# Kernel optimization log

Hardware: AMD Instinct MI355X
Metric: run time of the kernel (lower is better)

The kernel has to match this reference:

```python
import jax, jax.numpy as jnp
import numpy as np

B, T, E, H, FF = 8, 1024, 1024, 16, 4096
HD = E // H
SCALE = HD ** -0.5
EPS = 1e-12  # LayerNorm eps from TransformerLayer


def layer_norm(x, w, b):
    u = x.mean(-1, keepdims=True)
    s = ((x - u) ** 2).mean(-1, keepdims=True)  # biased variance, as in module
    return w * (x - u) / jnp.sqrt(s + EPS) + b


def setup_inputs() -> dict:
    key = jax.random.key(0)
    ks = jax.random.split(key, 8)
    std = 0.02  # nn.init.normal_(std=0.02)
    x = jax.random.normal(ks[0], (B, T, E), jnp.float32)
    # padding mask: positions >= length are padding (1 = ignore); ensure no all-masked row
    lengths = jax.random.randint(ks[1], (B,), T // 2, T + 1)
    self_padding_mask = jnp.arange(T)[None, :] >= lengths[:, None]
    # causal mask from SelfAttentionMask: triu(ones, 1)
    attn_mask = jnp.triu(jnp.ones((T, T), dtype=bool), 1)
    in_w = std * jax.random.normal(ks[2], (3 * E, E), jnp.float32)
    in_b = jnp.zeros((3 * E,), jnp.float32)
    out_w = std * jax.random.normal(ks[3], (E, E), jnp.float32)
    out_b = jnp.zeros((E,), jnp.float32)
    fc1_w = std * jax.random.normal(ks[4], (FF, E), jnp.float32)
    fc1_b = jnp.zeros((FF,), jnp.float32)
    fc2_w = std * jax.random.normal(ks[5], (E, FF), jnp.float32)
    fc2_b = jnp.zeros((E,), jnp.float32)
    ln1_w = jnp.ones((E,), jnp.float32)
    ln1_b = jnp.zeros((E,), jnp.float32)
    ln2_w = jnp.ones((E,), jnp.float32)
    ln2_b = jnp.zeros((E,), jnp.float32)
    return dict(x=x, in_w=in_w, in_b=in_b, out_w=out_w, out_b=out_b,
                fc1_w=fc1_w, fc1_b=fc1_b, fc2_w=fc2_w, fc2_b=fc2_b,
                ln1_w=ln1_w, ln1_b=ln1_b, ln2_w=ln2_w, ln2_b=ln2_b,
                self_padding_mask=self_padding_mask, attn_mask=attn_mask)


def reference(x, in_w, in_b, out_w, out_b, fc1_w, fc1_b, fc2_w, fc2_b,
              ln1_w, ln1_b, ln2_w, ln2_b, self_padding_mask, attn_mask):
    b, t, e = x.shape
    # --- self attention sublayer ---
    residual = x
    qkv = x @ in_w.T + in_b                       # [B,T,3E] fused in_proj (qkv_same path)
    q, k, v = jnp.split(qkv, 3, axis=-1)
    q = (q * SCALE).reshape(b, t, H, HD)
    k = k.reshape(b, t, H, HD)
    v = v.reshape(b, t, H, HD)
    scores = jnp.einsum('bqhd,bkhd->bhqk', q, k)  # [B,H,T,T]
    mask = attn_mask[None, None, :, :] | self_padding_mask[:, None, None, :]
    scores = jnp.where(mask, -jnp.inf, scores)
    p = jax.nn.softmax(scores, axis=-1)
    attn = jnp.einsum('bhqk,bkhd->bqhd', p, v).reshape(b, t, e)
    attn = attn @ out_w.T + out_b
    x = layer_norm(residual + attn, ln1_w, ln1_b)
    # --- feed-forward sublayer ---
    residual = x
    h = jax.nn.relu(x @ fc1_w.T + fc1_b)
    x = layer_norm(residual + (h @ fc2_w.T + fc2_b), ln2_w, ln2_b)
    return x
```

## Files before the change

### kernel.cpp

```cpp
#include <hip/hip_runtime.h>

typedef unsigned short u16;
typedef __attribute__((ext_vector_type(8))) short short8;
typedef __attribute__((ext_vector_type(4))) short short4v;
typedef __attribute__((ext_vector_type(4))) float f32x4;

#define DEV static __device__ __forceinline__

DEV float bf2f(u16 h) {
    union { unsigned int u; float f; } v; v.u = ((unsigned int)h) << 16; return v.f;
}
DEV u16 f2bf(float f) {
    union { float f; unsigned int u; } v; v.f = f;
    unsigned int r = (v.u + 0x7fff + ((v.u >> 16) & 1)) >> 16;
    return (u16)r;
}
DEV float ldx(const void* p, size_t i, int f32) {
    return f32 ? ((const float*)p)[i] : bf2f(((const u16*)p)[i]);
}

#define GLD16(g, l) __builtin_amdgcn_global_load_lds( \
    (const __attribute__((address_space(1))) void*)(g), \
    (__attribute__((address_space(3))) void*)(l), 16, 0, 0)

#define STAGE(P, pf32, eoff, dst8) do {                                        \
    if (!(pf32)) { GLD16(((const u16*)(P)) + (eoff), (dst8)); }                \
    else {                                                                     \
        const float* _p = ((const float*)(P)) + (eoff);                        \
        f32x4 _a = *(const f32x4*)_p, _b = *(const f32x4*)(_p + 4);            \
        short8 _s;                                                             \
        _s[0]=(short)f2bf(_a[0]); _s[1]=(short)f2bf(_a[1]);                    \
        _s[2]=(short)f2bf(_a[2]); _s[3]=(short)f2bf(_a[3]);                    \
        _s[4]=(short)f2bf(_b[0]); _s[5]=(short)f2bf(_b[1]);                    \
        _s[6]=(short)f2bf(_b[2]); _s[7]=(short)f2bf(_b[3]);                    \
        *(short8*)(dst8) = _s;                                                 \
    } } while (0)

__global__ __launch_bounds__(64) void probe_kernel(
    const void* __restrict__ x, const void* __restrict__ pad,
    int* __restrict__ flags, int* __restrict__ flagsA)
{
    const int lane = threadIdx.x;
    const u16* xu = (const u16*)x;
    const unsigned int e = (xu[lane * 2] >> 7) & 0xFF;
    const int sane = (e >= 0x70 && e <= 0x8F) ? 1 : 0;
    unsigned long long m = __ballot(sane);
    const int f32 = (__popcll(m) < 32) ? 1 : 0;

    const unsigned int* pi = (const unsigned int*)pad;
    int bytes = 0;
#pragma unroll
    for (int j = 0; j < 6; j++) {
        unsigned int v = pi[128 + j * 64 + lane];
        if (v > 1u) bytes = 1;
    }
    m = __ballot(bytes);
    if (lane == 0) {
        flags[0] = f32; flags[1] = (m != 0ULL) ? 1 : 0;
        flagsA[0] = 0;  flagsA[1] = 0;
    }
}

__global__ __launch_bounds__(256) void conv4(
    const void* __restrict__ src, u16* __restrict__ dst, int n4,
    const int* __restrict__ flags)
{
    const int i = blockIdx.x * 256 + threadIdx.x;
    if (i >= n4) return;
    if (flags[0]) {
        f32x4 v = ((const f32x4*)src)[i];
        short4v s;
        s[0] = (short)f2bf(v[0]); s[1] = (short)f2bf(v[1]);
        s[2] = (short)f2bf(v[2]); s[3] = (short)f2bf(v[3]);
        ((short4v*)dst)[i] = s;
    } else {
        ((short4v*)dst)[i] = ((const short4v*)src)[i];
    }
}

__global__ __launch_bounds__(256) void mask_to_bias(
    const void* __restrict__ pad, float* __restrict__ out,
    const int* __restrict__ flags)
{
    const int i = blockIdx.x * 256 + threadIdx.x;
    const int mv = flags[1] ? (int)((const unsigned char*)pad)[i]
                            : ((const int*)pad)[i];
    out[i] = mv ? -1e30f : 0.0f;
}

#define GEMM_CORE(Av, ASEL, a_row0, Wv, w_off, ldw, K)                        \
    __shared__ __align__(16) u16 As[128 * 32];                                \
    __shared__ __align__(16) u16 Bs[128 * 32];                                \
    const int inf32 = flags[0];                                               \
    const int af32  = (ASEL) ? inf32 : 0;                                     \
    const int tid  = threadIdx.x;                                             \
    const int lane = tid & 63;                                                \
    const int wave = tid >> 6;                                                \
    const int lc   = lane & 15;                                               \
    const int quad = lane >> 4;                                               \
    const int m0 = blockIdx.x * 128;                                          \
    const int n0 = blockIdx.y * 128;                                          \
    const int wm = (wave >> 1) * 64;                                          \
    const int wn = (wave & 1) * 64;                                           \
    const int r0 = tid >> 2;                                                  \
    const int ko = (tid & 3) * 8;                                             \
    f32x4 acc[4][4] = {};                                                     \
    for (int k0 = 0; k0 < (K); k0 += 32) {                                    \
        STAGE(Av, af32, ((size_t)(a_row0) + m0 + r0) * (K) + k0 + ko,         \
              &As[tid * 8]);                                                  \
        STAGE(Av, af32, ((size_t)(a_row0) + m0 + r0 + 64) * (K) + k0 + ko,    \
              &As[2048 + tid * 8]);                                           \
        STAGE(Wv, inf32, (size_t)(w_off) + (size_t)(n0 + r0) * (ldw) + k0 + ko,\
              &Bs[tid * 8]);                                                  \
        STAGE(Wv, inf32, (size_t)(w_off) + (size_t)(n0 + r0 + 64) * (ldw) + k0 + ko,\
              &Bs[2048 + tid * 8]);                                           \
        __syncthreads();                                                      \
        short8 afr[4], bfr[4];                                                \
        const int qd = quad * 8;                                              \
        _Pragma("unroll")                                                     \
        for (int mt = 0; mt < 4; mt++)                                        \
            afr[mt] = *(const short8*)&As[(wm + mt * 16 + lc) * 32 + qd];     \
        _Pragma("unroll")                                                     \
        for (int nt = 0; nt < 4; nt++)                                        \
            bfr[nt] = *(const short8*)&Bs[(wn + nt * 16 + lc) * 32 + qd];     \
        _Pragma("unroll")                                                     \
        for (int mt = 0; mt < 4; mt++)                                        \
            _Pragma("unroll")                                                 \
            for (int nt = 0; nt < 4; nt++)                                    \
                acc[mt][nt] = __builtin_amdgcn_mfma_f32_16x16x32_bf16(        \
                    afr[mt], bfr[nt], acc[mt][nt], 0, 0, 0);                  \
        __syncthreads();                                                      \
    }                                                                         \
    const int ce0 = n0 + wn + lc;                                             \
    const int re0 = m0 + wm + quad * 4;

template<int EPI>
__global__ __launch_bounds__(256, 2) void gemm_bt(
    const void* __restrict__ A, int a_sel, long a_row0,
    const void* __restrict__ W, long w_off,
    const void* __restrict__ bias, long b_off,
    const void* __restrict__ resid, int r_sel, long r_row0,
    u16* __restrict__ C, long c_row0,
    int N, int K, int ldw, const int* __restrict__ flags)
{
    GEMM_CORE(A, a_sel, a_row0, W, w_off, ldw, K)
    const int rf32 = r_sel ? inf32 : 0;
#pragma unroll
    for (int mt = 0; mt < 4; mt++) {
#pragma unroll
        for (int nt = 0; nt < 4; nt++) {
            const int c = ce0 + nt * 16;
            const float bv = ldx(bias, (size_t)b_off + c, inf32);
#pragma unroll
            for (int i = 0; i < 4; i++) {
                const int r = re0 + mt * 16 + i;
                float v = acc[mt][nt][i] + bv;
                if (EPI == 1)
                    v += ldx(resid, ((size_t)r_row0 + r) * N + c, rf32);
                if (EPI == 2) v = fmaxf(v, 0.0f);
                C[((size_t)c_row0 + r) * N + c] = f2bf(v);
            }
        }
    }
}

__global__ __launch_bounds__(256, 2) void gemm_qkv(
    const void* __restrict__ A, long a_row0,
    const void* __restrict__ W, const void* __restrict__ bias,
    u16* __restrict__ Qo, u16* __restrict__ Ko, u16* __restrict__ Vt,
    const int* __restrict__ flags)
{
    GEMM_CORE(A, 1, a_row0, W, 0, 1024, 1024)
    if (n0 < 1024) {
#pragma unroll
        for (int mt = 0; mt < 4; mt++)
#pragma unroll
            for (int nt = 0; nt < 4; nt++) {
                const int c = ce0 + nt * 16;
                const float bv = ldx(bias, c, inf32);
#pragma unroll
                for (int i = 0; i < 4; i++) {
                    const int r = re0 + mt * 16 + i;
                    Qo[((size_t)a_row0 + r) * 1024 + c] =
                        f2bf((acc[mt][nt][i] + bv) * 0.125f);
                }
            }
    } else if (n0 < 2048) {
#pragma unroll
        for (int mt = 0; mt < 4; mt++)
#pragma unroll
            for (int nt = 0; nt < 4; nt++) {
                const int c = ce0 + nt * 16;
                const float bv = ldx(bias, c, inf32);
#pragma unroll
                for (int i = 0; i < 4; i++) {
                    const int r = re0 + mt * 16 + i;
                    Ko[(size_t)r * 1024 + (c - 1024)] = f2bf(acc[mt][nt][i] + bv);
                }
            }
    } else {
#pragma unroll
        for (int mt = 0; mt < 4; mt++)
#pragma unroll
            for (int nt = 0; nt < 4; nt++) {
                const int c = ce0 + nt * 16;
                const float bv = ldx(bias, c, inf32);
                const int cv = c - 2048;
                const int hh = cv >> 6, d = cv & 63;
                const int rb = re0 + mt * 16;
                const int bl = rb >> 10, t = rb & 1023;
                short4v pk;
#pragma unroll
                for (int i = 0; i < 4; i++)
                    pk[i] = (short)f2bf(acc[mt][nt][i] + bv);
                *(short4v*)&Vt[((size_t)(bl * 16 + hh) * 64 + d) * 1024 + t] = pk;
            }
    }
}

__global__ __launch_bounds__(256, 2) void gemm_accf32(
    const void* __restrict__ A, const void* __restrict__ W, long w_off,
    const void* __restrict__ bias, const u16* __restrict__ resid, long r_row0,
    float* __restrict__ C, int ldw, int init, const int* __restrict__ flags)
{
    GEMM_CORE(A, 0, 0, W, w_off, ldw, 1024)
#pragma unroll
    for (int mt = 0; mt < 4; mt++) {
#pragma unroll
        for (int nt = 0; nt < 4; nt++) {
            const int c = ce0 + nt * 16;
            const float bv = ldx(bias, c, inf32);
#pragma unroll
            for (int i = 0; i < 4; i++) {
                const int r = re0 + mt * 16 + i;
                float v = acc[mt][nt][i];
                if (init) v += bv + bf2f(resid[((size_t)r_row0 + r) * 1024 + c]);
                else      v += C[(size_t)r * 1024 + c];
                C[(size_t)r * 1024 + c] = v;
            }
        }
    }
}

__global__ __launch_bounds__(256, 2) void attn_kernel(
    u16* __restrict__ QO, const u16* __restrict__ Ko,
    const u16* __restrict__ Vt, const float* __restrict__ kb, int b0)
{
    __shared__ __align__(16) u16 Qs[2 * 128 * 32];
    __shared__ __align__(16) u16 Ks[2][2 * 64 * 32];
    __shared__ __align__(16) u16 Vs[2][2 * 64 * 32];
    __shared__ __align__(16) u16 Ps[4][32 * 72];
    __shared__ float kba[1024];

    const int tid  = threadIdx.x;
    const int lane = tid & 63;
    const int w    = tid >> 6;
    const int lc   = lane & 15;
    const int quad = lane >> 4;
    const int bl = blockIdx.y >> 4;
    const int h  = blockIdx.y & 15;
    const int b  = b0 + bl;

    *(f32x4*)&kba[tid * 4] = *(const f32x4*)&kb[b * 1024 + tid * 4];

    for (int p = 0; p < 2; p++) {
        const int qt = p ? 7 - (int)blockIdx.x : (int)blockIdx.x;

#pragma unroll
        for (int it = 0; it < 4; it++) {
            const int kcd = it >> 1, half = it & 1;
            const int r = half * 64 + (tid >> 2);
            const int c = kcd * 32 + (tid & 3) * 8;
            GLD16(&QO[((size_t)(b * 1024 + qt * 128 + r)) * 1024 + h * 64 + c],
                  &Qs[kcd * 4096 + half * 2048 + tid * 8]);
        }
        {
            const int rr = tid >> 2;
#pragma unroll
            for (int it = 0; it < 2; it++) {
                const int cc = it * 32 + (tid & 3) * 8;
                GLD16(&Ko[((size_t)(bl * 1024 + rr)) * 1024 + h * 64 + cc],
                      &Ks[0][it * 2048 + tid * 8]);
                GLD16(&Vt[((size_t)(bl * 16 + h) * 64 + rr) * 1024 + cc],
                      &Vs[0][it * 2048 + tid * 8]);
            }
        }
        __syncthreads();

        short8 aq[2][2];
#pragma unroll
        for (int mt = 0; mt < 2; mt++)
#pragma unroll
            for (int kc = 0; kc < 2; kc++)
                aq[mt][kc] = *(const short8*)
                    &Qs[kc * 4096 + (w * 32 + mt * 16 + lc) * 32 + quad * 8];

        f32x4 o[2][4] = {};
        float m_i[2][4], l_i[2][4];
#pragma unroll
        for (int mt = 0; mt < 2; mt++)
#pragma unroll
            for (int i = 0; i < 4; i++) { m_i[mt][i] = -1e30f; l_i[mt][i] = 0.0f; }

        const int ktmax = 2 * qt + 2;
        for (int kt = 0; kt < ktmax; kt++) {
            const int cur = kt & 1;
            if (kt + 1 < ktmax) {
                const int nxt = cur ^ 1;
                const int rr = tid >> 2;
#pragma unroll
                for (int it = 0; it < 2; it++) {
                    const int cc = it * 32 + (tid & 3) * 8;
                    GLD16(&Ko[((size_t)(bl * 1024 + (kt + 1) * 64 + rr)) * 1024 + h * 64 + cc],
                          &Ks[nxt][it * 2048 + tid * 8]);
                    GLD16(&Vt[((size_t)(bl * 16 + h) * 64 + rr) * 1024 + (kt + 1) * 64 + cc],
                          &Vs[nxt][it * 2048 + tid * 8]);
                }
            }

            short8 bk[4][2];
#pragma unroll
            for (int nt = 0; nt < 4; nt++)
#pragma unroll
                for (int kc = 0; kc < 2; kc++)
                    bk[nt][kc] = *(const short8*)
                        &Ks[cur][kc * 2048 + (nt * 16 + lc) * 32 + quad * 8];

            f32x4 s[2][4];
#pragma unroll
            for (int mt = 0; mt < 2; mt++)
#pragma unroll
                for (int nt = 0; nt < 4; nt++) {
                    f32x4 z = {};
#pragma unroll
                    for (int kc = 0; kc < 2; kc++)
                        z = __builtin_amdgcn_mfma_f32_16x16x32_bf16(
                            aq[mt][kc], bk[nt][kc], z, 0, 0, 0);
                    s[mt][nt] = z;
                }

            const int causal = (kt >= 2 * qt);
            float al[2][4];
#pragma unroll
            for (int mt = 0; mt < 2; mt++) {
                const int qg0 = qt * 128 + w * 32 + mt * 16 + quad * 4;
#pragma unroll
                for (int nt = 0; nt < 4; nt++) {
                    const int kg = kt * 64 + nt * 16 + lc;
                    const float kbv = kba[kt * 64 + nt * 16 + lc];
#pragma unroll
                    for (int i = 0; i < 4; i++) {
                        float sv = s[mt][nt][i] + kbv;
                        if (causal && kg > qg0 + i) sv = -1e30f;
                        s[mt][nt][i] = sv;
                    }
                }
                float mnew[4], rs[4];
#pragma unroll
                for (int i = 0; i < 4; i++) {
                    float rm = fmaxf(fmaxf(s[mt][0][i], s[mt][1][i]),
                                     fmaxf(s[mt][2][i], s[mt][3][i]));
                    rm = fmaxf(rm, __shfl_xor(rm, 1));
                    rm = fmaxf(rm, __shfl_xor(rm, 2));
                    rm = fmaxf(rm, __shfl_xor(rm, 4));
                    rm = fmaxf(rm, __shfl_xor(rm, 8));
                    mnew[i] = fmaxf(m_i[mt][i], rm);
                    al[mt][i] = exp2f((m_i[mt][i] - mnew[i]) * 1.442695041f);
                    rs[i] = 0.0f;
                }
#pragma unroll
                for (int nt = 0; nt < 4; nt++)
#pragma unroll
                    for (int i = 0; i < 4; i++) {
                        float pp = exp2f((s[mt][nt][i] - mnew[i]) * 1.442695041f);
                        s[mt][nt][i] = pp;
                        rs[i] += pp;
                    }
#pragma unroll
                for (int i = 0; i < 4; i++) {
                    float r = rs[i];
                    r += __shfl_xor(r, 1);
                    r += __shfl_xor(r, 2);
                    r += __shfl_xor(r, 4);
                    r += __shfl_xor(r, 8);
                    l_i[mt][i] = l_i[mt][i] * al[mt][i] + r;
                    m_i[mt][i] = mnew[i];
                }
#pragma unroll
                for (int nt = 0; nt < 4; nt++)
#pragma unroll
                    for (int i = 0; i < 4; i++)
                        Ps[w][(mt * 16 + quad * 4 + i) * 72 + nt * 16 + lc] =
                            f2bf(s[mt][nt][i]);
            }

            short8 ap[2][2], bv2[4][2];
#pragma unroll
            for (int mt = 0; mt < 2; mt++)
#pragma unroll
                for (int kc = 0; kc < 2; kc++)
                    ap[mt][kc] = *(const short8*)
                        &Ps[w][(mt * 16 + lc) * 72 + kc * 32 + quad * 8];
#pragma unroll
            for (int nt = 0; nt < 4; nt++)
#pragma unroll
                for (int kc = 0; kc < 2; kc++)
                    bv2[nt][kc] = *(const short8*)
                        &Vs[cur][kc * 2048 + (nt * 16 + lc) * 32 + quad * 8];
#pragma unroll
            for (int mt = 0; mt < 2; mt++)
#pragma unroll
                for (int nt = 0; nt < 4; nt++) {
                    f32x4 oo = o[mt][nt];
#pragma unroll
                    for (int i = 0; i < 4; i++) oo[i] *= al[mt][i];
#pragma unroll
                    for (int kc = 0; kc < 2; kc++)
                        oo = __builtin_amdgcn_mfma_f32_16x16x32_bf16(
                            ap[mt][kc], bv2[nt][kc], oo, 0, 0, 0);
                    o[mt][nt] = oo;
                }
            __syncthreads();
        }

#pragma unroll
        for (int mt = 0; mt < 2; mt++)
#pragma unroll
            for (int i = 0; i < 4; i++) {
                const float inv = l_i[mt][i] > 0.0f ? 1.0f / l_i[mt][i] : 0.0f;
#pragma unroll
                for (int nt = 0; nt < 4; nt++) {
                    const int r = qt * 128 + w * 32 + mt * 16 + quad * 4 + i;
                    const int d = nt * 16 + lc;
                    QO[((size_t)(b * 1024 + r)) * 1024 + h * 64 + d] =
                        f2bf(o[mt][nt][i] * inv);
                }
            }
    }
}

template<int IN16, int OUTSEL>
__global__ __launch_bounds__(256) void ln_kernel(
    const void* __restrict__ yv, const void* __restrict__ w,
    const void* __restrict__ bb, void* __restrict__ o, long o_row0,
    const int* __restrict__ flags)
{
    const int row = blockIdx.x;
    const int tid = threadIdx.x;
    const int inf32 = flags[0];
    float x0, x1, x2, x3;
    if (IN16) {
        const u16* p = (const u16*)yv + (size_t)row * 1024 + tid * 4;
        short4v v = *(const short4v*)p;
        x0 = bf2f((u16)v[0]); x1 = bf2f((u16)v[1]);
        x2 = bf2f((u16)v[2]); x3 = bf2f((u16)v[3]);
    } else {
        const float* p = (const float*)yv + (size_t)row * 1024 + tid * 4;
        f32x4 v = *(const f32x4*)p;
        x0 = v[0]; x1 = v[1]; x2 = v[2]; x3 = v[3];
    }
    float s = x0 + x1 + x2 + x3;
    float q = x0 * x0 + x1 * x1 + x2 * x2 + x3 * x3;
#pragma unroll
    for (int off = 32; off; off >>= 1) {
        s += __shfl_xor(s, off);
        q += __shfl_xor(q, off);
    }
    __shared__ float sm[8];
    const int lane = tid & 63, wv = tid >> 6;
    if (lane == 0) { sm[wv] = s; sm[4 + wv] = q; }
    __syncthreads();
    const float ts = sm[0] + sm[1] + sm[2] + sm[3];
    const float tq = sm[4] + sm[5] + sm[6] + sm[7];
    const float mean = ts * (1.0f / 1024.0f);
    float var = tq * (1.0f / 1024.0f) - mean * mean;
    if (var < 0.0f) var = 0.0f;
    const float rinv = rsqrtf(var + 1e-12f);

    const size_t obase = ((size_t)o_row0 + row) * 1024 + tid * 4;
#pragma unroll
    for (int j = 0; j < 4; j++) {
        const int c = tid * 4 + j;
        float xv = (j == 0) ? x0 : (j == 1) ? x1 : (j == 2) ? x2 : x3;
        float v = ldx(w, c, inf32) * ((xv - mean) * rinv) + ldx(bb, c, inf32);
        if (OUTSEL && inf32) ((float*)o)[obase + j] = v;
        else                 ((u16*)o)[obase + j] = f2bf(v);
    }
}

extern "C" void kernel_launch(void* const* d_in, const int* in_sizes, int n_in,
                              void* d_out, int out_size, void* d_ws, size_t ws_size,
                              hipStream_t stream)
{
    const void* x     = d_in[0];
    const void* in_w  = d_in[1];
    const void* in_b  = d_in[2];
    const void* out_w = d_in[3];
    const void* out_b = d_in[4];
    const void* fc1_w = d_in[5];
    const void* fc1_b = d_in[6];
    const void* fc2_w = d_in[7];
    const void* fc2_b = d_in[8];
    const void* ln1w  = d_in[9];
    const void* ln1b  = d_in[10];
    const void* ln2w  = d_in[11];
    const void* ln2b  = d_in[12];
    const void* pad   = d_in[13];
    u16* outp = (u16*)d_out;
    char* ws = (char*)d_ws;
    dim3 blk(256);

    const size_t MB = 1024 * 1024;
    const bool bigWS = ws_size >= (105 * MB + 64 * 1024);

    if (bigWS) {
        u16*   xb   = (u16*)(ws + 0);
        u16*   x1   = (u16*)(ws + 0);
        u16*   w1b  = (u16*)(ws + 16 * MB);
        u16*   wob  = (u16*)(ws + 22 * MB);
        u16*   f1b  = (u16*)(ws + 24 * MB);
        u16*   f2b  = (u16*)(ws + 32 * MB);
        u16*   inbb = (u16*)(ws + 40 * MB);
        u16*   outbb= (u16*)(ws + 40 * MB + 8192);
        u16*   f1bb = (u16*)(ws + 40 * MB + 16384);
        u16*   f2bb = (u16*)(ws + 40 * MB + 24576);
        u16*   Ko   = (u16*)(ws + 41 * MB);
        u16*   Vt   = (u16*)(ws + 57 * MB);
        u16*   y1   = (u16*)(ws + 73 * MB);
        u16*   h    = (u16*)(ws + 41 * MB);
        u16*   y2   = (u16*)(ws + 16 * MB);
        int*   flags  = (int*)(ws + 105 * MB);
        int*   flagsA = (int*)(ws + 105 * MB + 32);
        float* kbias  = (float*)(ws + 105 * MB + 64);

        probe_kernel<<<dim3(1), dim3(64), 0, stream>>>(x, pad, flags, flagsA);
        mask_to_bias<<<dim3(32), blk, 0, stream>>>(pad, kbias, flags);
        conv4<<<dim3(8192), blk, 0, stream>>>(x, xb, 2097152, flags);
        conv4<<<dim3(3072), blk, 0, stream>>>(in_w, w1b, 786432, flags);
        conv4<<<dim3(1024), blk, 0, stream>>>(out_w, wob, 262144, flags);
        conv4<<<dim3(4096), blk, 0, stream>>>(fc1_w, f1b, 1048576, flags);
        conv4<<<dim3(4096), blk, 0, stream>>>(fc2_w, f2b, 1048576, flags);
        conv4<<<dim3(3), blk, 0, stream>>>(in_b, inbb, 768, flags);
        conv4<<<dim3(1), blk, 0, stream>>>(out_b, outbb, 256, flags);
        conv4<<<dim3(4), blk, 0, stream>>>(fc1_b, f1bb, 1024, flags);
        conv4<<<dim3(1), blk, 0, stream>>>(fc2_b, f2bb, 256, flags);

        gemm_qkv<<<dim3(64, 24), blk, 0, stream>>>(
            xb, 0, w1b, inbb, outp, Ko, Vt, flagsA);
        attn_kernel<<<dim3(4, 128), blk, 0, stream>>>(outp, Ko, Vt, kbias, 0);
        gemm_bt<1><<<dim3(64, 8), blk, 0, stream>>>(
            outp, 0, 0, wob, 0, outbb, 0, xb, 0, 0, y1, 0, 1024, 1024, 1024, flagsA);
        ln_kernel<1, 0><<<dim3(8192), blk, 0, stream>>>(y1, ln1w, ln1b, x1, 0, flags);
        gemm_bt<2><<<dim3(64, 32), blk, 0, stream>>>(
            x1, 0, 0, f1b, 0, f1bb, 0, nullptr, 0, 0, h, 0, 4096, 1024, 1024, flagsA);
        gemm_bt<1><<<dim3(64, 8), blk, 0, stream>>>(
            h, 0, 0, f2b, 0, f2bb, 0, x1, 0, 0, y2, 0, 1024, 4096, 4096, flagsA);
        ln_kernel<1, 1><<<dim3(8192), blk, 0, stream>>>(y2, ln2w, ln2b, d_out, 0, flags);
    } else {
        u16*   Ko    = (u16*)(ws + 0);
        u16*   Vt    = (u16*)(ws + 4 * MB);
        u16*   y1h   = (u16*)(ws + 0);
        float* acc   = (float*)(ws + 0);
        u16*   hc    = (u16*)(ws + 8 * MB);
        int*   flags  = (int*)(ws + 12 * MB);
        int*   flagsA = (int*)(ws + 12 * MB + 32);
        float* kbias  = (float*)(ws + 12 * MB + 64);

        probe_kernel<<<dim3(1), dim3(64), 0, stream>>>(x, pad, flags, flagsA);
        mask_to_bias<<<dim3(32), blk, 0, stream>>>(pad, kbias, flags);

        for (int q = 0; q < 4; q++) {
            const long r0 = (long)q * 2048;
            gemm_qkv<<<dim3(16, 24), blk, 0, stream>>>(
                x, r0, in_w, in_b, outp, Ko, Vt, flags);
            attn_kernel<<<dim3(4, 32), blk, 0, stream>>>(
                outp, Ko, Vt, kbias, q * 2);
        }
        for (int hf = 0; hf < 2; hf++) {
            const long r0 = (long)hf * 4096;
            gemm_bt<1><<<dim3(32, 8), blk, 0, stream>>>(
                outp, 0, r0, out_w, 0, out_b, 0, x, 1, r0,
                y1h, 0, 1024, 1024, 1024, flags);
            ln_kernel<1, 0><<<dim3(4096), blk, 0, stream>>>(
                y1h, ln1w, ln1b, outp, r0, flags);
        }
        for (int q = 3; q >= 0; q--) {
            const long r0 = (long)q * 2048;
            for (int c = 0; c < 4; c++) {
                gemm_bt<2><<<dim3(16, 8), blk, 0, stream>>>(
                    outp, 0, r0, fc1_w, (long)c * 1024 * 1024, fc1_b, (long)c * 1024,
                    nullptr, 0, 0, hc, 0, 1024, 1024, 1024, flags);
                gemm_accf32<<<dim3(16, 8), blk, 0, stream>>>(
                    hc, fc2_w, (long)c * 1024, fc2_b, outp, r0,
                    acc, 4096, c == 0, flags);
            }
            ln_kernel<0, 1><<<dim3(2048), blk, 0, stream>>>(
                acc, ln2w, ln2b, d_out, r0, flags);
        }
    }
}
```

Measured before the change: 611.2 us.

## Add 256x256-tile 8-wave pipelined GEMM for out-proj and FFN layers

Adds a new bf16 GEMM kernel with 512 threads, 256x256 output tiles, double-buffered direct global-to-LDS loads, swizzled LDS reads, barrier-interleaved MFMA phases and s_setprio scheduling. It replaces the previous 128-tile gemm_bt for the output projection and both FFN GEMMs on the big-workspace path. Larger tiles raise arithmetic intensity and cut global traffic, but the grid drops to 128 blocks for the N=1024 GEMMs, which may underfill the 256 CUs. The new kernel also ignores the dtype flags that gemm_bt took, so it assumes bf16 inputs.

After: 580.1 us. 5.1% less time.

```diff
diff --git a/kernel.cpp b/kernel.cpp
--- a/kernel.cpp
+++ b/kernel.cpp
@@ -242,6 +242,117 @@
     }
 }
 
+template<int EPI>
+__global__ __launch_bounds__(512, 2) void gemm8(
+    const u16* __restrict__ A, const u16* __restrict__ W,
+    const u16* __restrict__ bias, const u16* __restrict__ resid,
+    u16* __restrict__ C, int N, int K)
+{
+    __shared__ __align__(16) u16 As8[2][2][8192];
+    __shared__ __align__(16) u16 Bs8[2][2][8192];
+    const int tid  = threadIdx.x;
+    const int lane = tid & 63;
+    const int lc   = lane & 15;
+    const int quad = lane >> 4;
+    const int w    = tid >> 6;
+    const int wr   = w >> 2;
+    const int wc   = w & 3;
+    const int m0 = blockIdx.x * 256;
+    const int n0 = blockIdx.y * 256;
+
+    const int sr   = tid >> 2;
+    const int scol = ((((tid & 3) << 4) ^ (((tid >> 3) & 3) << 4)) >> 1);
+    const size_t aoff0 = (size_t)(m0 + sr) * K + scol;
+    const size_t aoff1 = (size_t)(m0 + 128 + sr) * K + scol;
+    const size_t boff0 = (size_t)(n0 + sr) * K + scol;
+    const size_t boff1 = (size_t)(n0 + 128 + sr) * K + scol;
+
+    const int fsw   = (quad ^ ((lc >> 1) & 3)) << 3;
+    const int aBase = (wr * 128 + lc) * 32 + fsw;
+    const int bBase = (wc * 64 + lc) * 32 + fsw;
+
+#define SA8(buf, kc, tb) do { \
+    GLD16(A + aoff0 + (tb) + (kc) * 32, &As8[buf][kc][tid * 8]); \
+    GLD16(A + aoff1 + (tb) + (kc) * 32, &As8[buf][kc][4096 + tid * 8]); } while (0)
+#define SB8(buf, kc, tb) do { \
+    GLD16(W + boff0 + (tb) + (kc) * 32, &Bs8[buf][kc][tid * 8]); \
+    GLD16(W + boff1 + (tb) + (kc) * 32, &Bs8[buf][kc][4096 + tid * 8]); } while (0)
+#define LDA4(KC, MH) do { _Pragma("unroll") \
+    for (int q_ = 0; q_ < 4; q_++) \
+        af[q_] = *(const short8*)&As8[c][KC][aBase + ((MH) * 4 + q_) * 512]; } while (0)
+#define LDB4(KC) do { _Pragma("unroll") \
+    for (int q_ = 0; q_ < 4; q_++) \
+        bf[q_] = *(const short8*)&Bs8[c][KC][bBase + q_ * 512]; } while (0)
+#define MFMA16(MH) do { _Pragma("unroll") \
+    for (int mq = 0; mq < 4; mq++) { _Pragma("unroll") \
+    for (int nq = 0; nq < 4; nq++) \
+        acc[(MH) * 4 + mq][nq] = __builtin_amdgcn_mfma_f32_16x16x32_bf16( \
+            af[mq], bf[nq], acc[(MH) * 4 + mq][nq], 0, 0, 0); } } while (0)
+#define BARW do { __builtin_amdgcn_s_barrier(); \
+    asm volatile("s_waitcnt lgkmcnt(0)" ::: "memory"); \
+    __builtin_amdgcn_s_setprio(1); } while (0)
+#define BARE do { __builtin_amdgcn_s_setprio(0); \
+    __builtin_amdgcn_s_barrier(); } while (0)
+
+    f32x4 acc[8][4] = {};
+    short8 af[4], bf[4];
+    const int NT = K >> 6;
+
+    SA8(0, 0, 0); SB8(0, 0, 0); SA8(0, 1, 0); SB8(0, 1, 0);
+    if (NT > 1) { SA8(1, 0, 64); SB8(1, 0, 64); }
+    if (NT > 1) asm volatile("s_waitcnt vmcnt(4)" ::: "memory");
+    else        asm volatile("s_waitcnt vmcnt(0)" ::: "memory");
+    __builtin_amdgcn_s_barrier();
+
+    for (int t = 0; t < NT; ++t) {
+        const int c = t & 1, nx = c ^ 1;
+        const int k0 = t << 6;
+        const bool s1 = (t + 1 < NT), s2 = (t + 2 < NT);
+        LDA4(0, 0); LDB4(0);
+        if (s1) SA8(nx, 1, k0 + 64);
+        BARW; MFMA16(0); BARE;
+        LDA4(0, 1);
+        if (s1) SB8(nx, 1, k0 + 64);
+        BARW; MFMA16(1); BARE;
+        LDA4(1, 0); LDB4(1);
+        if (s2) SA8(c, 0, k0 + 128);
+        BARW; MFMA16(0); BARE;
+        LDA4(1, 1);
+        if (s2) SB8(c, 0, k0 + 128);
+        BARW; MFMA16(1);
+        __builtin_amdgcn_s_setprio(0);
+        if (s2) asm volatile("s_waitcnt vmcnt(4)" ::: "memory");
+        else    asm volatile("s_waitcnt vmcnt(0)" ::: "memory");
+        __builtin_amdgcn_s_barrier();
+    }
+
+    const int cb0 = n0 + wc * 64 + lc;
+    const int rb0 = m0 + wr * 128 + quad * 4;
+#pragma unroll
+    for (int mt = 0; mt < 8; mt++) {
+#pragma unroll
+        for (int nt = 0; nt < 4; nt++) {
+            const int cN = cb0 + nt * 16;
+            const float bv = bf2f(bias[cN]);
+#pragma unroll
+            for (int i = 0; i < 4; i++) {
+                const int rM = rb0 + mt * 16 + i;
+                float v = acc[mt][nt][i] + bv;
+                if (EPI == 1) v += bf2f(resid[(size_t)rM * N + cN]);
+                if (EPI == 2) v = fmaxf(v, 0.0f);
+                C[(size_t)rM * N + cN] = f2bf(v);
+            }
+        }
+    }
+#undef SA8
+#undef SB8
+#undef LDA4
+#undef LDB4
+#undef MFMA16
+#undef BARW
+#undef BARE
+}
+
 __global__ __launch_bounds__(256, 2) void attn_kernel(
     u16* __restrict__ QO, const u16* __restrict__ Ko,
     const u16* __restrict__ Vt, const float* __restrict__ kb, int b0)
@@ -509,6 +620,7 @@
     u16* outp = (u16*)d_out;
     char* ws = (char*)d_ws;
     dim3 blk(256);
+    dim3 blk8(512);
 
     const size_t MB = 1024 * 1024;
     const bool bigWS = ws_size >= (105 * MB + 64 * 1024);
@@ -548,13 +660,13 @@
         gemm_qkv<<<dim3(64, 24), blk, 0, stream>>>(
             xb, 0, w1b, inbb, outp, Ko, Vt, flagsA);
         attn_kernel<<<dim3(4, 128), blk, 0, stream>>>(outp, Ko, Vt, kbias, 0);
-        gemm_bt<1><<<dim3(64, 8), blk, 0, stream>>>(
-            outp, 0, 0, wob, 0, outbb, 0, xb, 0, 0, y1, 0, 1024, 1024, 1024, flagsA);
+        gemm8<1><<<dim3(32, 4), blk8, 0, stream>>>(
+            outp, wob, outbb, xb, y1, 1024, 1024);
         ln_kernel<1, 0><<<dim3(8192), blk, 0, stream>>>(y1, ln1w, ln1b, x1, 0, flags);
-        gemm_bt<2><<<dim3(64, 32), blk, 0, stream>>>(
-            x1, 0, 0, f1b, 0, f1bb, 0, nullptr, 0, 0, h, 0, 4096, 1024, 1024, flagsA);
-        gemm_bt<1><<<dim3(64, 8), blk, 0, stream>>>(
-            h, 0, 0, f2b, 0, f2bb, 0, x1, 0, 0, y2, 0, 1024, 4096, 4096, flagsA);
+        gemm8<2><<<dim3(32, 16), blk8, 0, stream>>>(
+            x1, f1b, f1bb, nullptr, h, 4096, 1024);
+        gemm8<1><<<dim3(32, 4), blk8, 0, stream>>>(
+            h, f2b, f2bb, x1, y2, 1024, 4096);
         ln_kernel<1, 1><<<dim3(8192), blk, 0, stream>>>(y2, ln2w, ln2b, d_out, 0, flags);
     } else {
         u16*   Ko    = (u16*)(ws + 0);
```

## Add 512-thread 128x256 triple-buffered bf16 GEMM for projection and FFN layers

Applied to the files above, without the earlier changes.

Introduces a new GEMM kernel family (gemm8, gemm8_qkv) using 8 waves per block, a 128x256 output tile, 64-wide K steps and a three-stage LDS ring filled by direct global-to-LDS loads. Each K step is split into two half-steps: B-tile loads are interleaved with MFMA work, and s_setprio is raised around the MFMA bursts. The QKV, output-projection, FC1 and FC2 GEMMs in the large-workspace path are switched to these kernels, with epilogues for bias, residual, ReLU, Q scaling and V transpose. The larger tile is meant to raise data reuse and overlap loads with compute. In exchange it uses about 144KB of LDS per block, which limits occupancy, and it launches fewer blocks.

Result: faster. 531.7 us (-13.0%).

```diff
diff --git a/kernel.cpp b/kernel.cpp
--- a/kernel.cpp
+++ b/kernel.cpp
@@ -242,6 +242,166 @@
     }
 }
 
+#define GEMM8_PRE(Ag_, Wg_, Kg_)                                              \
+    __shared__ __align__(16) u16 Ab[3][128 * 64];                             \
+    __shared__ __align__(16) u16 Bb[3][256 * 64];                             \
+    const u16* Ag = (Ag_); const u16* Wg = (Wg_); const int Kg = (Kg_);       \
+    const int tid  = threadIdx.x;                                             \
+    const int lane = tid & 63;                                                \
+    const int lc   = lane & 15;                                               \
+    const int quad = lane >> 4;                                               \
+    const int w    = tid >> 6;                                                \
+    const int wr   = w >> 2;                                                  \
+    const int wc   = w & 3;                                                   \
+    const int m0 = blockIdx.x * 128;                                          \
+    const int n0 = blockIdx.y * 256;                                          \
+    const int srow = tid >> 3;                                                \
+    const int scol = (((tid & 7) ^ (srow & 7)) << 3);                         \
+    const int sw0 = (((quad) ^ (lc & 7)) << 3);                               \
+    const int sw1 = sw0 ^ 32;                                                 \
+    f32x4 acc[4][4] = {};                                                     \
+    short8 af[4], bf[4];
+
+#define SA8(buf, kk) do {                                                     \
+    GLD16(Ag + (size_t)(m0 + srow) * Kg + (kk) + scol, &Ab[buf][tid * 8]);    \
+    GLD16(Ag + (size_t)(m0 + 64 + srow) * Kg + (kk) + scol,                   \
+          &Ab[buf][4096 + tid * 8]); } while (0)
+#define SB8a(buf, kk) do {                                                    \
+    GLD16(Wg + (size_t)(n0 + srow) * Kg + (kk) + scol, &Bb[buf][tid * 8]);    \
+    GLD16(Wg + (size_t)(n0 + 64 + srow) * Kg + (kk) + scol,                   \
+          &Bb[buf][4096 + tid * 8]); } while (0)
+#define SB8b(buf, kk) do {                                                    \
+    GLD16(Wg + (size_t)(n0 + 128 + srow) * Kg + (kk) + scol,                  \
+          &Bb[buf][8192 + tid * 8]);                                          \
+    GLD16(Wg + (size_t)(n0 + 192 + srow) * Kg + (kk) + scol,                  \
+          &Bb[buf][12288 + tid * 8]); } while (0)
+#define LDFR(rbuf, SW) do { _Pragma("unroll")                                 \
+    for (int q_ = 0; q_ < 4; q_++) {                                          \
+        af[q_] = *(const short8*)&Ab[rbuf][(wr * 64 + q_ * 16 + lc) * 64 + (SW)];\
+        bf[q_] = *(const short8*)&Bb[rbuf][(wc * 64 + q_ * 16 + lc) * 64 + (SW)];\
+    } } while (0)
+#define MFMA16 do { _Pragma("unroll")                                         \
+    for (int mq = 0; mq < 4; mq++) { _Pragma("unroll")                        \
+    for (int nq = 0; nq < 4; nq++)                                            \
+        acc[mq][nq] = __builtin_amdgcn_mfma_f32_16x16x32_bf16(                \
+            af[mq], bf[nq], acc[mq][nq], 0, 0, 0); } } while (0)
+
+#define GEMM8_LOOP                                                            \
+    const int NT = Kg >> 6;                                                   \
+    SA8(0, 0); SB8a(0, 0); SB8b(0, 0);                                        \
+    if (NT > 1) { SA8(1, 64); SB8a(1, 64); SB8b(1, 64); }                     \
+    if (NT > 1) asm volatile("s_waitcnt vmcnt(6)" ::: "memory");              \
+    else        asm volatile("s_waitcnt vmcnt(0)" ::: "memory");              \
+    __builtin_amdgcn_s_barrier();                                             \
+    int rb_ = 0, wb_ = 2;                                                     \
+    for (int t = 0; t < NT; ++t) {                                            \
+        const bool s_ = (t + 2 < NT);                                         \
+        const int k2_ = (t + 2) << 6;                                         \
+        LDFR(rb_, sw0);                                                       \
+        if (s_) { SA8(wb_, k2_); SB8a(wb_, k2_); }                            \
+        __builtin_amdgcn_s_barrier();                                         \
+        asm volatile("s_waitcnt lgkmcnt(0)" ::: "memory");                    \
+        __builtin_amdgcn_s_setprio(1);                                        \
+        MFMA16;                                                               \
+        __builtin_amdgcn_s_setprio(0);                                        \
+        __builtin_amdgcn_s_barrier();                                         \
+        LDFR(rb_, sw1);                                                       \
+        if (s_) SB8b(wb_, k2_);                                               \
+        __builtin_amdgcn_s_barrier();                                         \
+        asm volatile("s_waitcnt lgkmcnt(0)" ::: "memory");                    \
+        __builtin_amdgcn_s_setprio(1);                                        \
+        MFMA16;                                                               \
+        __builtin_amdgcn_s_setprio(0);                                        \
+        if (s_) asm volatile("s_waitcnt vmcnt(6)" ::: "memory");              \
+        else    asm volatile("s_waitcnt vmcnt(0)" ::: "memory");              \
+        __builtin_amdgcn_s_barrier();                                         \
+        rb_ = (rb_ == 2) ? 0 : rb_ + 1;                                       \
+        wb_ = (wb_ == 2) ? 0 : wb_ + 1;                                       \
+    }                                                                         \
+    const int cb0 = n0 + wc * 64 + lc;                                        \
+    const int rb0 = m0 + wr * 64 + quad * 4;
+
+template<int EPI>
+__global__ __launch_bounds__(512, 2) void gemm8(
+    const u16* __restrict__ A, const u16* __restrict__ W,
+    const u16* __restrict__ bias, const u16* __restrict__ resid,
+    u16* __restrict__ C, int N, int K)
+{
+    GEMM8_PRE(A, W, K)
+    GEMM8_LOOP
+#pragma unroll
+    for (int mq = 0; mq < 4; mq++) {
+#pragma unroll
+        for (int nq = 0; nq < 4; nq++) {
+            const int cN = cb0 + nq * 16;
+            const float bv = bf2f(bias[cN]);
+#pragma unroll
+            for (int i = 0; i < 4; i++) {
+                const int rM = rb0 + mq * 16 + i;
+                float v = acc[mq][nq][i] + bv;
+                if (EPI == 1) v += bf2f(resid[(size_t)rM * N + cN]);
+                if (EPI == 2) v = fmaxf(v, 0.0f);
+                C[(size_t)rM * N + cN] = f2bf(v);
+            }
+        }
+    }
+}
+
+__global__ __launch_bounds__(512, 2) void gemm8_qkv(
+    const u16* __restrict__ A, const u16* __restrict__ W,
+    const u16* __restrict__ bias,
+    u16* __restrict__ Qo, u16* __restrict__ Ko, u16* __restrict__ Vt)
+{
+    GEMM8_PRE(A, W, 1024)
+    GEMM8_LOOP
+    if (n0 < 1024) {
+#pragma unroll
+        for (int mq = 0; mq < 4; mq++)
+#pragma unroll
+            for (int nq = 0; nq < 4; nq++) {
+                const int c = cb0 + nq * 16;
+                const float bv = bf2f(bias[c]);
+#pragma unroll
+                for (int i = 0; i < 4; i++) {
+                    const int r = rb0 + mq * 16 + i;
+                    Qo[(size_t)r * 1024 + c] =
+                        f2bf((acc[mq][nq][i] + bv) * 0.125f);
+                }
+            }
+    } else if (n0 < 2048) {
+#pragma unroll
+        for (int mq = 0; mq < 4; mq++)
+#pragma unroll
+            for (int nq = 0; nq < 4; nq++) {
+                const int c = cb0 + nq * 16;
+                const float bv = bf2f(bias[c]);
+#pragma unroll
+                for (int i = 0; i < 4; i++) {
+                    const int r = rb0 + mq * 16 + i;
+                    Ko[(size_t)r * 1024 + (c - 1024)] =
+                        f2bf(acc[mq][nq][i] + bv);
+                }
+            }
+    } else {
+#pragma unroll
+        for (int mq = 0; mq < 4; mq++)
+#pragma unroll
+            for (int nq = 0; nq < 4; nq++) {
+                const int c = cb0 + nq * 16;
+                const float bv = bf2f(bias[c]);
+                const int cv = c - 2048;
+                const int hh = cv >> 6, d = cv & 63;
+                const int rbase = rb0 + mq * 16;
+                const int bl = rbase >> 10, tt = rbase & 1023;
+                short4v pk;
+#pragma unroll
+                for (int i = 0; i < 4; i++)
+                    pk[i] = (short)f2bf(acc[mq][nq][i] + bv);
+                *(short4v*)&Vt[((size_t)(bl * 16 + hh) * 64 + d) * 1024 + tt] = pk;
+            }
+    }
+}
+
 __global__ __launch_bounds__(256, 2) void attn_kernel(
     u16* __restrict__ QO, const u16* __restrict__ Ko,
     const u16* __restrict__ Vt, const float* __restrict__ kb, int b0)
@@ -509,6 +669,7 @@
     u16* outp = (u16*)d_out;
     char* ws = (char*)d_ws;
     dim3 blk(256);
+    dim3 blk8(512);
 
     const size_t MB = 1024 * 1024;
     const bool bigWS = ws_size >= (105 * MB + 64 * 1024);
@@ -545,16 +706,16 @@
         conv4<<<dim3(4), blk, 0, stream>>>(fc1_b, f1bb, 1024, flags);
         conv4<<<dim3(1), blk, 0, stream>>>(fc2_b, f2bb, 256, flags);
 
-        gemm_qkv<<<dim3(64, 24), blk, 0, stream>>>(
-            xb, 0, w1b, inbb, outp, Ko, Vt, flagsA);
+        gemm8_qkv<<<dim3(64, 12), blk8, 0, stream>>>(
+            xb, w1b, inbb, outp, Ko, Vt);
         attn_kernel<<<dim3(4, 128), blk, 0, stream>>>(outp, Ko, Vt, kbias, 0);
-        gemm_bt<1><<<dim3(64, 8), blk, 0, stream>>>(
-            outp, 0, 0, wob, 0, outbb, 0, xb, 0, 0, y1, 0, 1024, 1024, 1024, flagsA);
+        gemm8<1><<<dim3(64, 4), blk8, 0, stream>>>(
+            outp, wob, outbb, xb, y1, 1024, 1024);
         ln_kernel<1, 0><<<dim3(8192), blk, 0, stream>>>(y1, ln1w, ln1b, x1, 0, flags);
-        gemm_bt<2><<<dim3(64, 32), blk, 0, stream>>>(
-            x1, 0, 0, f1b, 0, f1bb, 0, nullptr, 0, 0, h, 0, 4096, 1024, 1024, flagsA);
-        gemm_bt<1><<<dim3(64, 8), blk, 0, stream>>>(
-            h, 0, 0, f2b, 0, f2bb, 0, x1, 0, 0, y2, 0, 1024, 4096, 4096, flagsA);
+        gemm8<2><<<dim3(64, 16), blk8, 0, stream>>>(
+            x1, f1b, f1bb, nullptr, h, 4096, 1024);
+        gemm8<1><<<dim3(64, 4), blk8, 0, stream>>>(
+            h, f2b, f2bb, x1, y2, 1024, 4096);
         ln_kernel<1, 1><<<dim3(8192), blk, 0, stream>>>(y2, ln2w, ln2b, d_out, 0, flags);
     } else {
         u16*   Ko    = (u16*)(ws + 0);
```
